# Kernel optimization log

Hardware: AMD Instinct MI355X
Metric: run time of the kernel (lower is better)

## Reference

```python
import jax, jax.numpy as jnp
from jax import lax
import numpy as np

D = 1024      # input_size
H = D // 2    # proj hidden
T = 25        # num_ner_labels
B, S = 64, 512


def setup_inputs() -> dict:
    key = jax.random.key(0)
    ks = jax.random.split(key, 8)
    sc1 = 1.0 / np.sqrt(D)
    sc2 = 1.0 / np.sqrt(H)
    return {
        "encoder_out": jax.random.normal(ks[0], (B, S, D), dtype=jnp.float32),
        "W1": jax.random.uniform(ks[1], (D, H), jnp.float32, -sc1, sc1),
        "b1": jax.random.uniform(ks[2], (H,), jnp.float32, -sc1, sc1),
        "W2": jax.random.uniform(ks[3], (H, T), jnp.float32, -sc2, sc2),
        "b2": jax.random.uniform(ks[4], (T,), jnp.float32, -sc2, sc2),
        "start_trans": jax.random.uniform(ks[5], (T,), jnp.float32, -0.1, 0.1),
        "end_trans": jax.random.uniform(ks[6], (T,), jnp.float32, -0.1, 0.1),
        "trans": jax.random.uniform(ks[7], (T, T), jnp.float32, -0.1, 0.1),
        "ner_labels": jax.random.randint(jax.random.fold_in(key, 1), (B, S), 0, T, dtype=jnp.int64),
        "mask": jnp.ones((B, S), dtype=bool),
    }


def _crf_nll(emissions, start_trans, end_trans, trans, labels, mask):
    # torchcrf negative mean log-likelihood, batch_first
    maskf = mask.astype(emissions.dtype)
    # numerator: score of gold path
    em_at_tag = jnp.take_along_axis(emissions, labels[..., None], axis=2)[..., 0]  # [B,S]
    score0 = start_trans[labels[:, 0]] + em_at_tag[:, 0]
    trans_sc = trans[labels[:, :-1], labels[:, 1:]]                                # [B,S-1]
    step_score = (trans_sc + em_at_tag[:, 1:]) * maskf[:, 1:]
    last_idx = mask.sum(axis=1).astype(jnp.int32) - 1
    last_tag = jnp.take_along_axis(labels, last_idx[:, None].astype(labels.dtype), axis=1)[:, 0]
    numerator = score0 + step_score.sum(axis=1) + end_trans[last_tag]
    # denominator: log partition via forward algorithm (scan over time)
    alpha0 = start_trans[None, :] + emissions[:, 0]                                # [B,T]
    em_rest = jnp.swapaxes(emissions[:, 1:], 0, 1)                                 # [S-1,B,T]
    m_rest = jnp.swapaxes(mask[:, 1:], 0, 1)                                       # [S-1,B]

    def step(alpha, xs):
        em_t, m_t = xs
        new = jax.scipy.special.logsumexp(
            alpha[:, :, None] + trans[None, :, :] + em_t[:, None, :], axis=1)
        return jnp.where(m_t[:, None], new, alpha), None

    alpha, _ = lax.scan(step, alpha0, (em_rest, m_rest))
    log_Z = jax.scipy.special.logsumexp(alpha + end_trans[None, :], axis=1)        # [B]
    return -jnp.mean(numerator - log_Z)


def reference(encoder_out, W1, b1, W2, b2, start_trans, end_trans, trans, ner_labels, mask):
    h = jax.nn.gelu(encoder_out @ W1 + b1, approximate=False)  # dropout is eval-mode identity
    emissions = h @ W2 + b2                                    # [B,S,T]
    return _crf_nll(emissions, start_trans, end_trans, trans, ner_labels, mask)
```

## Files before the change

kernel.cpp:

```cpp
#include <hip/hip_runtime.h>
#include <math.h>

#define DD 1024
#define HH 512
#define TT 25
#define BB 64
#define SS 512
#define MM (BB*SS)
#define NC 32

typedef __attribute__((ext_vector_type(8))) short short8;
typedef __attribute__((ext_vector_type(4))) float floatx4;
typedef __attribute__((ext_vector_type(16))) float floatx16;

static __device__ __forceinline__ unsigned short f2bf(float f) {
  unsigned u = __float_as_uint(f);
  u = (u + 0x7FFFu + ((u >> 16) & 1u)) >> 16;
  return (unsigned short)u;
}
static __device__ __forceinline__ float bf2f(unsigned short s) {
  return __uint_as_float(((unsigned)s) << 16);
}
static __device__ __forceinline__ float rl(float v, int i) {
  return __int_as_float(__builtin_amdgcn_readlane(__float_as_int(v), i));
}
static __device__ __forceinline__ void load_lds16(const void* g, void* l) {
  __builtin_amdgcn_global_load_lds(
      (const __attribute__((address_space(1))) unsigned int*)g,
      (__attribute__((address_space(3))) unsigned int*)l, 16, 0, 0);
}
union U4S8 { uint4 u; short8 s; };

__global__ __launch_bounds__(256) void k_prep(
    const float* __restrict__ W1, const float* __restrict__ W2,
    unsigned short* __restrict__ W1T2, unsigned short* __restrict__ W2p) {
  const int t = threadIdx.x;
  if (blockIdx.y < 8) {
    __shared__ unsigned short tile[64 * 72];
    const int k0 = blockIdx.x * 64, n0 = blockIdx.y * 64;
    #pragma unroll
    for (int it = 0; it < 16; it++) {
      int idx = t + it * 256;
      int kk = idx >> 6, nn = idx & 63;
      tile[nn * 72 + kk] = f2bf(W1[(size_t)(k0 + kk) * HH + n0 + nn]);
    }
    __syncthreads();
    #pragma unroll
    for (int it = 0; it < 4; it++) {
      int idx = (t + it * 256) * 4;
      int nn = idx >> 6, kk = idx & 63;
      ushort4 v;
      v.x = tile[nn * 72 + kk];     v.y = tile[nn * 72 + kk + 1];
      v.z = tile[nn * 72 + kk + 2]; v.w = tile[nn * 72 + kk + 3];
      int kt = (k0 >> 5) + (kk >> 5), kkk = kk & 31;
      *(ushort4*)(W1T2 + (size_t)kt * (HH * 32) + (n0 + nn) * 32 + kkk) = v;
    }
  } else {
    #pragma unroll
    for (int e = 0; e < 4; e++) {
      int idx = blockIdx.x * 1024 + t + e * 256;
      int row = idx >> 9, k = idx & 511;
      float v = (row < TT) ? W2[(size_t)k * TT + row] : 0.f;
      W2p[(size_t)row * HH + k] = f2bf(v);
    }
  }
}

__global__ __launch_bounds__(256, 4) void k_emis(
    const float* __restrict__ X, const unsigned short* __restrict__ W1T2,
    const float* __restrict__ b1, const unsigned short* __restrict__ W2p,
    const float* __restrict__ b2, float* __restrict__ em) {
  __shared__ __attribute__((aligned(16))) short lds[18432];

  const int tid  = threadIdx.x;
  const int lane = tid & 63;
  const int w    = tid >> 6;
  const int l15  = lane & 15;
  const int kc   = lane >> 4;
  const int m0   = blockIdx.x * 64;
  const int colbase = blockIdx.y * 256;

  floatx4 acc[4][4];
  #pragma unroll
  for (int a = 0; a < 4; a++)
    #pragma unroll
    for (int b = 0; b < 4; b++)
      acc[a][b] = (floatx4){0.f, 0.f, 0.f, 0.f};

  const int am = tid >> 2;
  const int ac = tid & 3;
  const float* Xrow = X + (size_t)(m0 + am) * DD + ac * 8;

  const unsigned short* gW = W1T2 + (size_t)(colbase + w * 64) * 32 + lane * 8;

  {
    short* lW = lds + 2048 + w * 2048;
    #pragma unroll
    for (int j = 0; j < 4; j++)
      load_lds16(gW + j * 512, lW + j * 512);
  }
  float4 yv0 = *(const float4*)(Xrow);
  float4 yv1 = *(const float4*)(Xrow + 4);

  for (int t = 0; t < 32; ++t) {
    short* sBc = lds + 2048 + (t & 1) * 8192;

    float4 zv0, zv1;
    if (t < 31) {
      short* lW = lds + 2048 + ((t + 1) & 1) * 8192 + w * 2048;
      const unsigned short* g = gW + (size_t)(t + 1) * (HH * 32);
      #pragma unroll
      for (int j = 0; j < 4; j++)
        load_lds16(g + j * 512, lW + j * 512);
      zv0 = *(const float4*)(Xrow + (t + 1) * 32);
      zv1 = *(const float4*)(Xrow + (t + 1) * 32 + 4);
    }

    {
      unsigned p0 = (unsigned)f2bf(yv0.x) | ((unsigned)f2bf(yv0.y) << 16);
      unsigned p1 = (unsigned)f2bf(yv0.z) | ((unsigned)f2bf(yv0.w) << 16);
      unsigned p2 = (unsigned)f2bf(yv1.x) | ((unsigned)f2bf(yv1.y) << 16);
      unsigned p3 = (unsigned)f2bf(yv1.z) | ((unsigned)f2bf(yv1.w) << 16);
      *(uint4*)(lds + am * 32 + ac * 8) = make_uint4(p0, p1, p2, p3);
    }
    if (t < 31) { yv0 = zv0; yv1 = zv1; }

    asm volatile("s_waitcnt vmcnt(6) lgkmcnt(0)" ::: "memory");
    __builtin_amdgcn_s_barrier();
    asm volatile("" ::: "memory");

    short8 af[4], bfr[4];
    #pragma unroll
    for (int mt = 0; mt < 4; mt++)
      af[mt] = *(const short8*)(lds + (mt * 16 + l15) * 32 + kc * 8);
    #pragma unroll
    for (int nt = 0; nt < 4; nt++)
      bfr[nt] = *(const short8*)(sBc + (w * 64 + nt * 16 + l15) * 32 + kc * 8);
    asm volatile("s_waitcnt lgkmcnt(0)" ::: "memory");
    __builtin_amdgcn_sched_barrier(0);
    #pragma unroll
    for (int mt = 0; mt < 4; mt++)
      #pragma unroll
      for (int nt = 0; nt < 4; nt++)
        acc[mt][nt] = __builtin_amdgcn_mfma_f32_16x16x32_bf16(af[mt], bfr[nt], acc[mt][nt], 0, 0, 0);

    asm volatile("" ::: "memory");
    __builtin_amdgcn_s_barrier();
    asm volatile("" ::: "memory");
  }

  short* sH = lds;
  float* sC = (float*)(lds + 8448);
  const int mt_g = w & 1, kh_g = w >> 1;

  short8 w2f[2][4];
  #pragma unroll
  for (int nt2 = 0; nt2 < 2; nt2++)
    #pragma unroll
    for (int ks = 0; ks < 4; ks++)
      w2f[nt2][ks] = *(const short8*)(W2p + (size_t)(nt2 * 16 + l15) * HH
                                      + colbase + kh_g * 128 + ks * 32 + kc * 8);

  #pragma unroll
  for (int half = 0; half < 2; half++) {
    __syncthreads();
    #pragma unroll
    for (int mt2 = 0; mt2 < 2; mt2++) {
      int mt = half * 2 + mt2;
      #pragma unroll
      for (int nt = 0; nt < 4; nt++) {
        int n = w * 64 + nt * 16 + l15;
        float bias = b1[colbase + n];
        #pragma unroll
        for (int r = 0; r < 4; r++) {
          int ml = mt2 * 16 + kc * 4 + r;
          float v = acc[mt][nt][r] + bias;
          float g = 0.5f * v * (1.0f + erff(v * 0.70710678118654752f));
          sH[ml * 264 + n] = (short)f2bf(g);
        }
      }
    }
    __syncthreads();
    #pragma unroll
    for (int nt2 = 0; nt2 < 2; nt2++) {
      floatx4 c2 = (floatx4){0.f, 0.f, 0.f, 0.f};
      #pragma unroll
      for (int ks = 0; ks < 4; ks++) {
        short8 a2 = *(const short8*)(sH + (mt_g * 16 + l15) * 264 + kh_g * 128 + ks * 32 + kc * 8);
        c2 = __builtin_amdgcn_mfma_f32_16x16x32_bf16(a2, w2f[nt2][ks], c2, 0, 0, 0);
      }
      #pragma unroll
      for (int r = 0; r < 4; r++)
        sC[kh_g * 1024 + (mt_g * 16 + kc * 4 + r) * 32 + nt2 * 16 + l15] = c2[r];
    }
    __syncthreads();
    for (int o = tid; o < 32 * TT; o += 256) {
      int m = o / TT, t = o % TT;
      float val = sC[m * 32 + t] + sC[1024 + m * 32 + t];
      if (blockIdx.y == 0) val += b2[t];
      atomicAdd(em + (size_t)(m0 + half * 32 + m) * TT + t, val);
    }
  }
}

__global__ __launch_bounds__(64) void k_chunk(
    const float* __restrict__ em, const float* __restrict__ trans,
    float* __restrict__ Mats) {
  const int b = blockIdx.x, c = blockIdx.y;
  const int lane = threadIdx.x;
  const int h = lane >> 5;
  const int n = lane & 31;
  const float* emb = em + (size_t)b * SS * TT;

  unsigned a1p[4], a2p[4];
  #pragma unroll
  for (int p = 0; p < 4; p++) {
    int i0 = h * 8 + 2 * p, i1 = i0 + 1;
    unsigned lo = (n < TT && i0 < TT) ? (unsigned)f2bf(__expf(trans[i0 * TT + n])) : 0u;
    unsigned hi = (n < TT && i1 < TT) ? (unsigned)f2bf(__expf(trans[i1 * TT + n])) : 0u;
    a1p[p] = lo | (hi << 16);
    int j0 = 16 + h * 8 + 2 * p, j1 = j0 + 1;
    lo = (n < TT && j0 < TT) ? (unsigned)f2bf(__expf(trans[j0 * TT + n])) : 0u;
    hi = (n < TT && j1 < TT) ? (unsigned)f2bf(__expf(trans[j1 * TT + n])) : 0u;
    a2p[p] = lo | (hi << 16);
  }
  U4S8 A1, A2;
  A1.u = make_uint4(a1p[0], a1p[1], a1p[2], a1p[3]);
  A2.u = make_uint4(a2p[0], a2p[1], a2p[2], a2p[3]);

  unsigned bp1[4], bp2[4];
  #pragma unroll
  for (int p = 0; p < 4; p++) {
    int k0 = h * 8 + 2 * p;
    bp1[p] = ((k0 == n) ? 0x3F80u : 0u) | ((k0 + 1 == n) ? 0x3F800000u : 0u);
    int k2 = 16 + h * 8 + 2 * p;
    bp2[p] = ((k2 == n) ? 0x3F80u : 0u) | ((k2 + 1 == n) ? 0x3F800000u : 0u);
  }

  const int s0 = 1 + c * 16;
  const int nst = (s0 + 16 <= SS) ? 16 : (SS - s0);

  float emv[16], f[16];
  #pragma unroll
  for (int e = 0; e < 16; e++) {
    int r = (e & 3) + 8 * (e >> 2) + 4 * h;
    emv[e] = (r < TT) ? emb[s0 * TT + r] : 0.f;
  }

  for (int t = 0; t < nst; t++) {
    const float rs = (t == 8) ? 32.0f : 0.0f;
    float ex[16];
    #pragma unroll
    for (int e = 0; e < 16; e++) ex[e] = __expf(emv[e] - rs);
    int sn = (s0 + t + 1 < SS) ? s0 + t + 1 : SS - 1;
    #pragma unroll
    for (int e = 0; e < 16; e++) {
      int r = (e & 3) + 8 * (e >> 2) + 4 * h;
      emv[e] = (r < TT) ? emb[sn * TT + r] : 0.f;
    }
    U4S8 B1, B2;
    B1.u = make_uint4(bp1[0], bp1[1], bp1[2], bp1[3]);
    B2.u = make_uint4(bp2[0], bp2[1], bp2[2], bp2[3]);
    floatx16 D = __builtin_amdgcn_mfma_f32_32x32x16_bf16(A1.s, B1.s,
                   __builtin_amdgcn_mfma_f32_32x32x16_bf16(A2.s, B2.s,
                     (floatx16){0.f,0.f,0.f,0.f,0.f,0.f,0.f,0.f,
                                0.f,0.f,0.f,0.f,0.f,0.f,0.f,0.f}, 0,0,0), 0,0,0);
    #pragma unroll
    for (int e = 0; e < 16; e++) f[e] = D[e] * ex[e];
    if (t == nst - 1) break;
    unsigned P[16];
    #pragma unroll
    for (int p = 0; p < 8; p++)
      P[p] = (unsigned)f2bf(f[2 * p]) | ((unsigned)f2bf(f[2 * p + 1]) << 16);
    unsigned sp[8];
    #pragma unroll
    for (int p = 0; p < 8; p++)
      sp[p] = (unsigned)__shfl_xor((int)P[p], 32);
    bool up = (h == 1);
    bp1[0] = up ? sp[2] : P[0];
    bp1[1] = up ? sp[3] : P[1];
    bp1[2] = up ? P[2] : sp[0];
    bp1[3] = up ? P[3] : sp[1];
    bp2[0] = up ? sp[6] : P[4];
    bp2[1] = up ? sp[7] : P[5];
    bp2[2] = up ? P[6] : sp[4];
    bp2[3] = up ? P[7] : sp[5];
  }

  if (n < TT) {
    float* Mc = Mats + ((size_t)(b * NC + c)) * (TT * TT) + n * TT;
    #pragma unroll
    for (int e = 0; e < 16; e++) {
      int r = (e & 3) + 8 * (e >> 2) + 4 * h;
      if (r < TT) Mc[r] = __logf(f[e]) + 32.0f;
    }
  }
}

__global__ __launch_bounds__(64) void k_comb(
    const float* __restrict__ em, const float* __restrict__ start,
    const float* __restrict__ endt, const float* __restrict__ trans,
    const int* __restrict__ labels, const float* __restrict__ Mats,
    float* __restrict__ partial) {
  const int b = blockIdx.x;
  const int tid = threadIdx.x;
  const float* emb = em + (size_t)b * SS * TT;
  const int* lab = labels + b * SS;

  float part = 0.f;
  for (int s = tid; s < SS; s += 64) {
    int l = lab[s];
    if (s == 0) part += start[l] + emb[l];
    else        part += trans[lab[s - 1] * TT + l] + emb[s * TT + l];
  }
  #pragma unroll
  for (int off = 32; off; off >>= 1) part += __shfl_xor(part, off);
  float num = part + endt[lab[SS - 1]];

  const int jj = (tid < TT) ? tid : 0;
  float a = (tid < TT) ? start[tid] + emb[tid] : -1e30f;
  const float* Mb = Mats + (size_t)b * NC * (TT * TT);
  for (int c = 0; c < NC; c++) {
    const float* Mc = Mb + c * (TT * TT);
    float col[TT];
    float mxc = -1e30f;
    #pragma unroll
    for (int i = 0; i < TT; i++) {
      col[i] = Mc[i * TT + jj];
      mxc = fmaxf(mxc, col[i]);
    }
    float a0 = __builtin_amdgcn_readfirstlane(a);
    float p = __expf(a - a0);
    float d0 = 0.f, d1 = 0.f, d2 = 0.f, d3 = 0.f;
    #pragma unroll
    for (int i = 0; i < 24; i += 4) {
      d0 = fmaf(rl(p, i + 0), __expf(col[i + 0] - mxc), d0);
      d1 = fmaf(rl(p, i + 1), __expf(col[i + 1] - mxc), d1);
      d2 = fmaf(rl(p, i + 2), __expf(col[i + 2] - mxc), d2);
      d3 = fmaf(rl(p, i + 3), __expf(col[i + 3] - mxc), d3);
    }
    d0 = fmaf(rl(p, 24), __expf(col[24] - mxc), d0);
    float anew = a0 + mxc + __logf((d0 + d1) + (d2 + d3));
    a = (tid < TT) ? anew : -1e30f;
  }

  float v = (tid < TT) ? a + endt[tid] : -1e30f;
  float mx = v;
  #pragma unroll
  for (int off = 16; off; off >>= 1) mx = fmaxf(mx, __shfl_xor(mx, off, 32));
  float e = (tid < TT) ? __expf(v - mx) : 0.f;
  #pragma unroll
  for (int off = 16; off; off >>= 1) e += __shfl_xor(e, off, 32);
  if (tid == 0) partial[b] = (mx + __logf(e)) - num;
}

__global__ void k_final(const float* __restrict__ partial, float* __restrict__ out) {
  int tid = threadIdx.x;
  float v = partial[tid];
  #pragma unroll
  for (int off = 32; off; off >>= 1) v += __shfl_xor(v, off);
  if (tid == 0) out[0] = v * (1.0f / 64.0f);
}

extern "C" void kernel_launch(void* const* d_in, const int* in_sizes, int n_in,
                              void* d_out, int out_size, void* d_ws, size_t ws_size,
                              hipStream_t stream) {
  const float* X   = (const float*)d_in[0];
  const float* W1  = (const float*)d_in[1];
  const float* b1  = (const float*)d_in[2];
  const float* W2  = (const float*)d_in[3];
  const float* b2  = (const float*)d_in[4];
  const float* st  = (const float*)d_in[5];
  const float* en  = (const float*)d_in[6];
  const float* tr  = (const float*)d_in[7];
  const int* labels = (const int*)d_in[8];

  char* ws = (char*)d_ws;
  unsigned short* W1T2 = (unsigned short*)ws;
  unsigned short* W2p  = (unsigned short*)(ws + 0x100000);
  float* em            = (float*)(ws + 0x110000);
  float* Mats          = (float*)(ws + 0x430000);
  float* partial       = (float*)(ws + 0x930000);

  k_prep <<<dim3(16, 9), 256, 0, stream>>>(W1, W2, W1T2, W2p);
  hipMemsetAsync(em, 0, (size_t)MM * TT * sizeof(float), stream);
  k_emis <<<dim3(512, 2), 256, 0, stream>>>(X, W1T2, b1, W2p, b2, em);
  k_chunk<<<dim3(BB, NC), 64, 0, stream>>>(em, tr, Mats);
  k_comb <<<BB, 64, 0, stream>>>(em, st, en, tr, labels, Mats, partial);
  k_final<<<1, 64, 0, stream>>>(partial, (float*)d_out);
}
```

Baseline: 303.3 us.

## Load X fragments directly into registers and XOR-swizzle W1 LDS tiles

```diff
diff --git a/kernel.cpp b/kernel.cpp
--- a/kernel.cpp
+++ b/kernel.cpp
@@ -18,9 +18,6 @@
   u = (u + 0x7FFFu + ((u >> 16) & 1u)) >> 16;
   return (unsigned short)u;
 }
-static __device__ __forceinline__ float bf2f(unsigned short s) {
-  return __uint_as_float(((unsigned)s) << 16);
-}
 static __device__ __forceinline__ float rl(float v, int i) {
   return __int_as_float(__builtin_amdgcn_readlane(__float_as_int(v), i));
 }
@@ -53,7 +50,10 @@
       v.x = tile[nn * 72 + kk];     v.y = tile[nn * 72 + kk + 1];
       v.z = tile[nn * 72 + kk + 2]; v.w = tile[nn * 72 + kk + 3];
       int kt = (k0 >> 5) + (kk >> 5), kkk = kk & 31;
-      *(ushort4*)(W1T2 + (size_t)kt * (HH * 32) + (n0 + nn) * 32 + kkk) = v;
+      int n = n0 + nn;
+      size_t slice = (size_t)kt * (HH * 32) + (size_t)(n & ~63) * 32;
+      int o = ((((n & 63) * 64) + ((kkk >> 3) * 16)) ^ ((n & 7) << 4)) + (kkk & 7) * 2;
+      *(ushort4*)((char*)W1T2 + slice * 2 + o) = v;
     }
   } else {
     #pragma unroll
@@ -66,11 +66,11 @@
   }
 }
 
-__global__ __launch_bounds__(256, 4) void k_emis(
+__global__ __launch_bounds__(256, 3) void k_emis(
     const float* __restrict__ X, const unsigned short* __restrict__ W1T2,
     const float* __restrict__ b1, const unsigned short* __restrict__ W2p,
     const float* __restrict__ b2, float* __restrict__ em) {
-  __shared__ __attribute__((aligned(16))) short lds[18432];
+  __shared__ __attribute__((aligned(16))) short lds[16640];
 
   const int tid  = threadIdx.x;
   const int lane = tid & 63;
@@ -87,66 +87,70 @@
     for (int b = 0; b < 4; b++)
       acc[a][b] = (floatx4){0.f, 0.f, 0.f, 0.f};
 
-  const int am = tid >> 2;
-  const int ac = tid & 3;
-  const float* Xrow = X + (size_t)(m0 + am) * DD + ac * 8;
+  const float* Xa[4];
+  #pragma unroll
+  for (int mt = 0; mt < 4; mt++)
+    Xa[mt] = X + (size_t)(m0 + mt * 16 + l15) * DD + kc * 8;
 
   const unsigned short* gW = W1T2 + (size_t)(colbase + w * 64) * 32 + lane * 8;
 
+  float4 xc[8];
+  #pragma unroll
+  for (int mt = 0; mt < 4; mt++) {
+    xc[2 * mt]     = *(const float4*)(Xa[mt]);
+    xc[2 * mt + 1] = *(const float4*)(Xa[mt] + 4);
+  }
   {
-    short* lW = lds + 2048 + w * 2048;
+    short* lW = lds + w * 2048;
     #pragma unroll
     for (int j = 0; j < 4; j++)
       load_lds16(gW + j * 512, lW + j * 512);
   }
-  float4 yv0 = *(const float4*)(Xrow);
-  float4 yv1 = *(const float4*)(Xrow + 4);
+
+  const int swz = ((l15 & 7) << 4);
 
   for (int t = 0; t < 32; ++t) {
-    short* sBc = lds + 2048 + (t & 1) * 8192;
-
-    float4 zv0, zv1;
+    short8 af[4];
+    #pragma unroll
+    for (int mt = 0; mt < 4; mt++) {
+      const float4 a = xc[2 * mt], b = xc[2 * mt + 1];
+      unsigned q0 = (unsigned)f2bf(a.x) | ((unsigned)f2bf(a.y) << 16);
+      unsigned q1 = (unsigned)f2bf(a.z) | ((unsigned)f2bf(a.w) << 16);
+      unsigned q2 = (unsigned)f2bf(b.x) | ((unsigned)f2bf(b.y) << 16);
+      unsigned q3 = (unsigned)f2bf(b.z) | ((unsigned)f2bf(b.w) << 16);
+      U4S8 u; u.u = make_uint4(q0, q1, q2, q3);
+      af[mt] = u.s;
+    }
+
     if (t < 31) {
-      short* lW = lds + 2048 + ((t + 1) & 1) * 8192 + w * 2048;
+      #pragma unroll
+      for (int mt = 0; mt < 4; mt++) {
+        xc[2 * mt]     = *(const float4*)(Xa[mt] + (t + 1) * 32);
+        xc[2 * mt + 1] = *(const float4*)(Xa[mt] + (t + 1) * 32 + 4);
+      }
+      short* lW = lds + ((t + 1) & 1) * 8192 + w * 2048;
       const unsigned short* g = gW + (size_t)(t + 1) * (HH * 32);
       #pragma unroll
       for (int j = 0; j < 4; j++)
         load_lds16(g + j * 512, lW + j * 512);
-      zv0 = *(const float4*)(Xrow + (t + 1) * 32);
-      zv1 = *(const float4*)(Xrow + (t + 1) * 32 + 4);
-    }
-
-    {
-      unsigned p0 = (unsigned)f2bf(yv0.x) | ((unsigned)f2bf(yv0.y) << 16);
-      unsigned p1 = (unsigned)f2bf(yv0.z) | ((unsigned)f2bf(yv0.w) << 16);
-      unsigned p2 = (unsigned)f2bf(yv1.x) | ((unsigned)f2bf(yv1.y) << 16);
-      unsigned p3 = (unsigned)f2bf(yv1.z) | ((unsigned)f2bf(yv1.w) << 16);
-      *(uint4*)(lds + am * 32 + ac * 8) = make_uint4(p0, p1, p2, p3);
-    }
-    if (t < 31) { yv0 = zv0; yv1 = zv1; }
-
-    asm volatile("s_waitcnt vmcnt(6) lgkmcnt(0)" ::: "memory");
-    __builtin_amdgcn_s_barrier();
-    asm volatile("" ::: "memory");
-
-    short8 af[4], bfr[4];
-    #pragma unroll
-    for (int mt = 0; mt < 4; mt++)
-      af[mt] = *(const short8*)(lds + (mt * 16 + l15) * 32 + kc * 8);
-    #pragma unroll
-    for (int nt = 0; nt < 4; nt++)
-      bfr[nt] = *(const short8*)(sBc + (w * 64 + nt * 16 + l15) * 32 + kc * 8);
-    asm volatile("s_waitcnt lgkmcnt(0)" ::: "memory");
-    __builtin_amdgcn_sched_barrier(0);
+      asm volatile("s_waitcnt vmcnt(12)" ::: "memory");
+    } else {
+      asm volatile("s_waitcnt vmcnt(0)" ::: "memory");
+    }
+
+    const char* sBb = (const char*)lds + (t & 1) * 16384;
+    short8 bfr[4];
+    #pragma unroll
+    for (int nt = 0; nt < 4; nt++) {
+      int row = w * 64 + nt * 16 + l15;
+      int off = ((row * 64) + kc * 16) ^ swz;
+      bfr[nt] = *(const short8*)(sBb + off);
+    }
     #pragma unroll
     for (int mt = 0; mt < 4; mt++)
       #pragma unroll
       for (int nt = 0; nt < 4; nt++)
         acc[mt][nt] = __builtin_amdgcn_mfma_f32_16x16x32_bf16(af[mt], bfr[nt], acc[mt][nt], 0, 0, 0);
-
-    asm volatile("" ::: "memory");
-    __builtin_amdgcn_s_barrier();
-    asm volatile("" ::: "memory");
   }
 
   short* sH = lds;
```

Measured after the change: 385.9 us. +27.2%, slower.

## Load W1 fragments directly to registers and double-buffer swizzled X tile in LDS

Applied to the files above, without the earlier changes.

```diff
diff --git a/kernel.cpp b/kernel.cpp
--- a/kernel.cpp
+++ b/kernel.cpp
@@ -18,22 +18,14 @@
   u = (u + 0x7FFFu + ((u >> 16) & 1u)) >> 16;
   return (unsigned short)u;
 }
-static __device__ __forceinline__ float bf2f(unsigned short s) {
-  return __uint_as_float(((unsigned)s) << 16);
-}
 static __device__ __forceinline__ float rl(float v, int i) {
   return __int_as_float(__builtin_amdgcn_readlane(__float_as_int(v), i));
 }
-static __device__ __forceinline__ void load_lds16(const void* g, void* l) {
-  __builtin_amdgcn_global_load_lds(
-      (const __attribute__((address_space(1))) unsigned int*)g,
-      (__attribute__((address_space(3))) unsigned int*)l, 16, 0, 0);
-}
 union U4S8 { uint4 u; short8 s; };
 
 __global__ __launch_bounds__(256) void k_prep(
     const float* __restrict__ W1, const float* __restrict__ W2,
-    unsigned short* __restrict__ W1T2, unsigned short* __restrict__ W2p) {
+    unsigned short* __restrict__ W1T3, unsigned short* __restrict__ W2p) {
   const int t = threadIdx.x;
   if (blockIdx.y < 8) {
     __shared__ unsigned short tile[64 * 72];
@@ -46,14 +38,16 @@
     }
     __syncthreads();
     #pragma unroll
-    for (int it = 0; it < 4; it++) {
-      int idx = (t + it * 256) * 4;
-      int nn = idx >> 6, kk = idx & 63;
-      ushort4 v;
-      v.x = tile[nn * 72 + kk];     v.y = tile[nn * 72 + kk + 1];
-      v.z = tile[nn * 72 + kk + 2]; v.w = tile[nn * 72 + kk + 3];
-      int kt = (k0 >> 5) + (kk >> 5), kkk = kk & 31;
-      *(ushort4*)(W1T2 + (size_t)kt * (HH * 32) + (n0 + nn) * 32 + kkk) = v;
+    for (int it = 0; it < 2; it++) {
+      int u = t + it * 256;
+      int nn = u >> 3, kk8 = u & 7;
+      uint4 v = *(const uint4*)&tile[nn * 72 + kk8 * 8];
+      int n = n0 + nn;
+      int kt = (k0 >> 5) + (kk8 >> 2);
+      int kc = kk8 & 3;
+      int lanei = kc * 16 + (n & 15);
+      size_t dst = (((size_t)kt * 32 + (n >> 4)) * 64 + lanei) * 8;
+      *(uint4*)(W1T3 + dst) = v;
     }
   } else {
     #pragma unroll
@@ -66,11 +60,11 @@
   }
 }
 
-__global__ __launch_bounds__(256, 4) void k_emis(
-    const float* __restrict__ X, const unsigned short* __restrict__ W1T2,
+__global__ __launch_bounds__(256, 3) void k_emis(
+    const float* __restrict__ X, const unsigned short* __restrict__ W1T3,
     const float* __restrict__ b1, const unsigned short* __restrict__ W2p,
     const float* __restrict__ b2, float* __restrict__ em) {
-  __shared__ __attribute__((aligned(16))) short lds[18432];
+  __shared__ __attribute__((aligned(16))) short lds[16640];
 
   const int tid  = threadIdx.x;
   const int lane = tid & 63;
@@ -90,63 +84,69 @@
   const int am = tid >> 2;
   const int ac = tid & 3;
   const float* Xrow = X + (size_t)(m0 + am) * DD + ac * 8;
-
-  const unsigned short* gW = W1T2 + (size_t)(colbase + w * 64) * 32 + lane * 8;
-
-  {
-    short* lW = lds + 2048 + w * 2048;
-    #pragma unroll
-    for (int j = 0; j < 4; j++)
-      load_lds16(gW + j * 512, lW + j * 512);
-  }
+  const int xwb = (am * 64 + ac * 16) ^ ((am & 7) << 4);
+
+  const unsigned short* gW = W1T3
+      + (((size_t)(colbase >> 4) + w * 4) * 64 + lane) * 8;
+
   float4 yv0 = *(const float4*)(Xrow);
   float4 yv1 = *(const float4*)(Xrow + 4);
+  short8 wf[4];
+  #pragma unroll
+  for (int nt = 0; nt < 4; nt++)
+    wf[nt] = *(const short8*)(gW + nt * 512);
+  {
+    unsigned p0 = (unsigned)f2bf(yv0.x) | ((unsigned)f2bf(yv0.y) << 16);
+    unsigned p1 = (unsigned)f2bf(yv0.z) | ((unsigned)f2bf(yv0.w) << 16);
+    unsigned p2 = (unsigned)f2bf(yv1.x) | ((unsigned)f2bf(yv1.y) << 16);
+    unsigned p3 = (unsigned)f2bf(yv1.z) | ((unsigned)f2bf(yv1.w) << 16);
+    *(uint4*)((char*)lds + xwb) = make_uint4(p0, p1, p2, p3);
+  }
+  yv0 = *(const float4*)(Xrow + 32);
+  yv1 = *(const float4*)(Xrow + 36);
+  asm volatile("s_waitcnt lgkmcnt(0)" ::: "memory");
+  __builtin_amdgcn_s_barrier();
+  asm volatile("" ::: "memory");
 
   for (int t = 0; t < 32; ++t) {
-    short* sBc = lds + 2048 + (t & 1) * 8192;
-
-    float4 zv0, zv1;
+    const char* sXc = (const char*)lds + (t & 1) * 4096;
+
+    short8 af[4];
+    #pragma unroll
+    for (int mt = 0; mt < 4; mt++) {
+      int row = mt * 16 + l15;
+      af[mt] = *(const short8*)(sXc + ((row * 64 + kc * 16) ^ ((l15 & 7) << 4)));
+    }
+
+    short8 wf2[4];
     if (t < 31) {
-      short* lW = lds + 2048 + ((t + 1) & 1) * 8192 + w * 2048;
-      const unsigned short* g = gW + (size_t)(t + 1) * (HH * 32);
-      #pragma unroll
-      for (int j = 0; j < 4; j++)
-        load_lds16(g + j * 512, lW + j * 512);
-      zv0 = *(const float4*)(Xrow + (t + 1) * 32);
-      zv1 = *(const float4*)(Xrow + (t + 1) * 32 + 4);
-    }
-
-    {
+      #pragma unroll
+      for (int nt = 0; nt < 4; nt++)
+        wf2[nt] = *(const short8*)(gW + (size_t)(t + 1) * 16384 + nt * 512);
       unsigned p0 = (unsigned)f2bf(yv0.x) | ((unsigned)f2bf(yv0.y) << 16);
       unsigned p1 = (unsigned)f2bf(yv0.z) | ((unsigned)f2bf(yv0.w) << 16);
       unsigned p2 = (unsigned)f2bf(yv1.x) | ((unsigned)f2bf(yv1.y) << 16);
       unsigned p3 = (unsigned)f2bf(yv1.z) | ((unsigned)f2bf(yv1.w) << 16);
-      *(uint4*)(lds + am * 32 + ac * 8) = make_uint4(p0, p1, p2, p3);
-    }
-    if (t < 31) { yv0 = zv0; yv1 = zv1; }
-
-    asm volatile("s_waitcnt vmcnt(6) lgkmcnt(0)" ::: "memory");
-    __builtin_amdgcn_s_barrier();
-    asm volatile("" ::: "memory");
-
-    short8 af[4], bfr[4];
+      *(uint4*)((char*)lds + (((t + 1) & 1) * 4096) + xwb) = make_uint4(p0, p1, p2, p3);
+      if (t < 30) {
+        yv0 = *(const float4*)(Xrow + (t + 2) * 32);
+        yv1 = *(const float4*)(Xrow + (t + 2) * 32 + 4);
+      }
+    }
+
     #pragma unroll
     for (int mt = 0; mt < 4; mt++)
-      af[mt] = *(const short8*)(lds + (mt * 16 + l15) * 32 + kc * 8);
-    #pragma unroll
-    for (int nt = 0; nt < 4; nt++)
-      bfr[nt] = *(const short8*)(sBc + (w * 64 + nt * 16 + l15) * 32 + kc * 8);
-    asm volatile("s_waitcnt lgkmcnt(0)" ::: "memory");
-    __builtin_amdgcn_sched_barrier(0);
-    #pragma unroll
-    for (int mt = 0; mt < 4; mt++)
       #pragma unroll
       for (int nt = 0; nt < 4; nt++)
-        acc[mt][nt] = __builtin_amdgcn_mfma_f32_16x16x32_bf16(af[mt], bfr[nt], acc[mt][nt], 0, 0, 0);
-
-    asm volatile("" ::: "memory");
-    __builtin_amdgcn_s_barrier();
-    asm volatile("" ::: "memory");
+        acc[mt][nt] = __builtin_amdgcn_mfma_f32_16x16x32_bf16(af[mt], wf[nt], acc[mt][nt], 0, 0, 0);
+
+    if (t < 31) {
+      #pragma unroll
+      for (int nt = 0; nt < 4; nt++) wf[nt] = wf2[nt];
+      asm volatile("s_waitcnt lgkmcnt(0)" ::: "memory");
+      __builtin_amdgcn_s_barrier();
+      asm volatile("" ::: "memory");
+    }
   }
 
   short* sH = lds;
@@ -376,15 +376,15 @@
   const int* labels = (const int*)d_in[8];
 
   char* ws = (char*)d_ws;
-  unsigned short* W1T2 = (unsigned short*)ws;
+  unsigned short* W1T3 = (unsigned short*)ws;
   unsigned short* W2p  = (unsigned short*)(ws + 0x100000);
   float* em            = (float*)(ws + 0x110000);
   float* Mats          = (float*)(ws + 0x430000);
   float* partial       = (float*)(ws + 0x930000);
 
-  k_prep <<<dim3(16, 9), 256, 0, stream>>>(W1, W2, W1T2, W2p);
+  k_prep <<<dim3(16, 9), 256, 0, stream>>>(W1, W2, W1T3, W2p);
   hipMemsetAsync(em, 0, (size_t)MM * TT * sizeof(float), stream);
-  k_emis <<<dim3(512, 2), 256, 0, stream>>>(X, W1T2, b1, W2p, b2, em);
+  k_emis <<<dim3(512, 2), 256, 0, stream>>>(X, W1T3, b1, W2p, b2, em);
   k_chunk<<<dim3(BB, NC), 64, 0, stream>>>(em, tr, Mats);
   k_comb <<<BB, 64, 0, stream>>>(em, st, en, tr, labels, Mats, partial);
   k_final<<<1, 64, 0, stream>>>(partial, (float*)d_out);
```

Measured after the change: 330.2 us. +8.9%, slower.

## XOR-swizzle LDS tiles for A/B fragments and deepen X register prefetch

Applied to the files above, without the earlier changes.

```diff
diff --git a/kernel.cpp b/kernel.cpp
--- a/kernel.cpp
+++ b/kernel.cpp
@@ -18,9 +18,6 @@
   u = (u + 0x7FFFu + ((u >> 16) & 1u)) >> 16;
   return (unsigned short)u;
 }
-static __device__ __forceinline__ float bf2f(unsigned short s) {
-  return __uint_as_float(((unsigned)s) << 16);
-}
 static __device__ __forceinline__ float rl(float v, int i) {
   return __int_as_float(__builtin_amdgcn_readlane(__float_as_int(v), i));
 }
@@ -53,7 +50,10 @@
       v.x = tile[nn * 72 + kk];     v.y = tile[nn * 72 + kk + 1];
       v.z = tile[nn * 72 + kk + 2]; v.w = tile[nn * 72 + kk + 3];
       int kt = (k0 >> 5) + (kk >> 5), kkk = kk & 31;
-      *(ushort4*)(W1T2 + (size_t)kt * (HH * 32) + (n0 + nn) * 32 + kkk) = v;
+      int n = n0 + nn;
+      size_t slice = (size_t)kt * (HH * 32) + (size_t)(n & ~63) * 32;
+      int o = ((((n & 63) * 64) + ((kkk >> 3) * 16)) ^ ((n & 7) << 4)) + (kkk & 7) * 2;
+      *(ushort4*)((char*)W1T2 + slice * 2 + o) = v;
     }
   } else {
     #pragma unroll
@@ -90,6 +90,7 @@
   const int am = tid >> 2;
   const int ac = tid & 3;
   const float* Xrow = X + (size_t)(m0 + am) * DD + ac * 8;
+  const int xwb = (am * 64 + ac * 16) ^ ((am & 7) << 4);
 
   const unsigned short* gW = W1T2 + (size_t)(colbase + w * 64) * 32 + lane * 8;
 
@@ -99,43 +100,57 @@
     for (int j = 0; j < 4; j++)
       load_lds16(gW + j * 512, lW + j * 512);
   }
-  float4 yv0 = *(const float4*)(Xrow);
-  float4 yv1 = *(const float4*)(Xrow + 4);
+  float4 xa0 = *(const float4*)(Xrow);
+  float4 xa1 = *(const float4*)(Xrow + 4);
+  float4 xb0 = *(const float4*)(Xrow + 32);
+  float4 xb1 = *(const float4*)(Xrow + 36);
 
   for (int t = 0; t < 32; ++t) {
     short* sBc = lds + 2048 + (t & 1) * 8192;
 
-    float4 zv0, zv1;
+    float4 xc0, xc1;
     if (t < 31) {
       short* lW = lds + 2048 + ((t + 1) & 1) * 8192 + w * 2048;
       const unsigned short* g = gW + (size_t)(t + 1) * (HH * 32);
       #pragma unroll
       for (int j = 0; j < 4; j++)
         load_lds16(g + j * 512, lW + j * 512);
-      zv0 = *(const float4*)(Xrow + (t + 1) * 32);
-      zv1 = *(const float4*)(Xrow + (t + 1) * 32 + 4);
+    }
+    if (t < 30) {
+      xc0 = *(const float4*)(Xrow + (t + 2) * 32);
+      xc1 = *(const float4*)(Xrow + (t + 2) * 32 + 4);
     }
 
     {
-      unsigned p0 = (unsigned)f2bf(yv0.x) | ((unsigned)f2bf(yv0.y) << 16);
-      unsigned p1 = (unsigned)f2bf(yv0.z) | ((unsigned)f2bf(yv0.w) << 16);
-      unsigned p2 = (unsigned)f2bf(yv1.x) | ((unsigned)f2bf(yv1.y) << 16);
-      unsigned p3 = (unsigned)f2bf(yv1.z) | ((unsigned)f2bf(yv1.w) << 16);
-      *(uint4*)(lds + am * 32 + ac * 8) = make_uint4(p0, p1, p2, p3);
-    }
-    if (t < 31) { yv0 = zv0; yv1 = zv1; }
-
-    asm volatile("s_waitcnt vmcnt(6) lgkmcnt(0)" ::: "memory");
+      unsigned p0 = (unsigned)f2bf(xa0.x) | ((unsigned)f2bf(xa0.y) << 16);
+      unsigned p1 = (unsigned)f2bf(xa0.z) | ((unsigned)f2bf(xa0.w) << 16);
+      unsigned p2 = (unsigned)f2bf(xa1.x) | ((unsigned)f2bf(xa1.y) << 16);
+      unsigned p3 = (unsigned)f2bf(xa1.z) | ((unsigned)f2bf(xa1.w) << 16);
+      *(uint4*)((char*)lds + xwb) = make_uint4(p0, p1, p2, p3);
+    }
+    xa0 = xb0; xa1 = xb1;
+    if (t < 30) { xb0 = xc0; xb1 = xc1; }
+
+    if (t < 31) {
+      asm volatile("s_waitcnt vmcnt(6) lgkmcnt(0)" ::: "memory");
+    } else {
+      asm volatile("s_waitcnt vmcnt(0) lgkmcnt(0)" ::: "memory");
+    }
     __builtin_amdgcn_s_barrier();
     asm volatile("" ::: "memory");
 
     short8 af[4], bfr[4];
     #pragma unroll
-    for (int mt = 0; mt < 4; mt++)
-      af[mt] = *(const short8*)(lds + (mt * 16 + l15) * 32 + kc * 8);
-    #pragma unroll
-    for (int nt = 0; nt < 4; nt++)
-      bfr[nt] = *(const short8*)(sBc + (w * 64 + nt * 16 + l15) * 32 + kc * 8);
+    for (int mt = 0; mt < 4; mt++) {
+      int row = mt * 16 + l15;
+      af[mt] = *(const short8*)((char*)lds + ((row * 64 + kc * 16) ^ ((l15 & 7) << 4)));
+    }
+    #pragma unroll
+    for (int nt = 0; nt < 4; nt++) {
+      int rloc = nt * 16 + l15;
+      int off = (rloc * 64 + kc * 16) ^ ((l15 & 7) << 4);
+      bfr[nt] = *(const short8*)((char*)(sBc + w * 2048) + off);
+    }
     asm volatile("s_waitcnt lgkmcnt(0)" ::: "memory");
     __builtin_amdgcn_sched_barrier(0);
     #pragma unroll
```

Result: no change. 304.8 us (+0.5%).
